# Kernel tuning notes

Hardware: AMD Instinct MI355X
Metric: run time of the kernel (lower is better)

## Reference

```python
import jax, jax.numpy as jnp
import numpy as np

B, CH, N = 4, 128, 4096
PC = CH // 2  # pos channels = 64


def setup_inputs() -> dict:
    key = jax.random.key(0)
    ks = jax.random.split(key, 6)
    s_p = 1.0 / np.sqrt(PC)
    s_v = 1.0 / np.sqrt(CH)
    return {
        "pos_bot": jax.random.normal(ks[0], (B, PC, N), dtype=jnp.float32),
        "corr_feats": jax.random.normal(ks[1], (B, CH, N), dtype=jnp.float32),
        "Wp": jax.random.uniform(ks[2], (PC, PC), jnp.float32, -s_p, s_p),
        "bp": jax.random.uniform(ks[3], (PC,), jnp.float32, -s_p, s_p),
        "Wv": jax.random.uniform(ks[4], (CH, CH), jnp.float32, -s_v, s_v),
        "bv": jax.random.uniform(ks[5], (CH,), jnp.float32, -s_v, s_v),
        "beta": jnp.asarray([1.0], dtype=jnp.float32),
    }


def reference(pos_bot, corr_feats, Wp, bp, Wv, bv, beta):
    # 1x1 Conv1d == per-position matmul over channels
    pos = jnp.einsum("oc,bcn->bon", Wp, pos_bot) + bp[None, :, None]      # [B,64,N]
    value = jnp.einsum("oc,bcn->bon", Wv, corr_feats) + bv[None, :, None]  # [B,128,N]

    x = jnp.transpose(pos, (0, 2, 1))  # [B,N,64]
    # squared euclidean pairwise distance: ||xi||^2 + ||xj||^2 - 2 xi.xj
    sq = jnp.sum(x * x, axis=-1)  # [B,N]
    d2 = sq[:, :, None] + sq[:, None, :] - 2.0 * jnp.einsum("bnd,bmd->bnm", x, x)
    d2 = jnp.maximum(d2, 0.0)
    kernel = jnp.exp(-d2 * beta[0])  # [B,N,N] Gaussian RBF

    equation_F = jnp.transpose(value, (0, 2, 1))  # [B,N,128]
    return kernel, equation_F
```

## Files before the change

kernel.cpp:

```cpp
#include <hip/hip_runtime.h>
#include <hip/hip_bf16.h>

typedef _Float16 f16x8 __attribute__((ext_vector_type(8)));
typedef _Float16 f16x4 __attribute__((ext_vector_type(4)));
typedef float    f32x4 __attribute__((ext_vector_type(4)));

constexpr int BB = 4;
constexpr int CH = 128;
constexpr int PC = 64;
constexpr int NN = 4096;

__global__ __launch_bounds__(256) void proj_pos_kernel(
    const float* __restrict__ pos_bot,
    const float* __restrict__ Wp,
    const float* __restrict__ bp,
    _Float16* __restrict__ xbuf,
    float*    __restrict__ sq)
{
    const int tid  = threadIdx.x;
    const int wid  = tid >> 6;
    const int lane = tid & 63;
    const int l15  = lane & 15;
    const int lg   = lane >> 4;
    const int b    = blockIdx.y;
    const int n    = blockIdx.x * 16 + l15;
    const int mt   = wid;

    f16x8 wf[2], pb[2];
#pragma unroll
    for (int ks = 0; ks < 2; ++ks) {
        const float* wp = Wp + (mt * 16 + l15) * PC + ks * 32 + lg * 8;
        f32x4 w0 = *reinterpret_cast<const f32x4*>(wp);
        f32x4 w1 = *reinterpret_cast<const f32x4*>(wp + 4);
        f16x8 f;
#pragma unroll
        for (int e = 0; e < 4; ++e) { f[e] = (_Float16)w0[e]; f[e + 4] = (_Float16)w1[e]; }
        wf[ks] = f;
        f16x8 g;
#pragma unroll
        for (int e = 0; e < 8; ++e) {
            const int c = ks * 32 + lg * 8 + e;
            g[e] = (_Float16)pos_bot[((size_t)(b * PC + c)) * NN + n];
        }
        pb[ks] = g;
    }

    f32x4 acc = {0.f, 0.f, 0.f, 0.f};
    acc = __builtin_amdgcn_mfma_f32_16x16x32_f16(wf[0], pb[0], acc, 0, 0, 0);
    acc = __builtin_amdgcn_mfma_f32_16x16x32_f16(wf[1], pb[1], acc, 0, 0, 0);

    float partial = 0.f;
    f16x4 h4;
#pragma unroll
    for (int r = 0; r < 4; ++r) {
        const int o = mt * 16 + lg * 4 + r;
        const float v = acc[r] + bp[o];
        const _Float16 h = (_Float16)v;
        h4[r] = h;
        const float hf = (float)h;
        partial = fmaf(hf, hf, partial);
    }
    *reinterpret_cast<f16x4*>(xbuf + ((size_t)(b * NN + n)) * PC + mt * 16 + lg * 4) = h4;

    partial += __shfl_xor(partial, 16);
    partial += __shfl_xor(partial, 32);
    __shared__ float psum[4][16];
    if (lane < 16) psum[wid][l15] = partial;
    __syncthreads();
    if (tid < 16)
        sq[b * NN + blockIdx.x * 16 + tid] =
            psum[0][tid] + psum[1][tid] + psum[2][tid] + psum[3][tid];
}

__global__ __launch_bounds__(256) void gram_kernel(
    const _Float16* __restrict__ xbuf,
    const float*    __restrict__ sq,
    const float*    __restrict__ beta,
    float*          __restrict__ out,
    const float*    __restrict__ corr,
    const float*    __restrict__ Wv,
    const float*    __restrict__ bv,
    float*          __restrict__ eqF)
{
    const int tid  = threadIdx.x;
    const int wid  = tid >> 6;
    const int lane = tid & 63;
    const int l15  = lane & 15;
    const int lg   = lane >> 4;

    if (blockIdx.z == BB) {
        const int blk = blockIdx.y * 32 + blockIdx.x;
        const int b   = blk >> 8;
        const int n   = (blk & 255) * 16 + l15;

        f16x8 cb[4];
#pragma unroll
        for (int ks = 0; ks < 4; ++ks) {
            f16x8 g;
#pragma unroll
            for (int e = 0; e < 8; ++e) {
                const int c = ks * 32 + lg * 8 + e;
                g[e] = (_Float16)corr[((size_t)(b * CH + c)) * NN + n];
            }
            cb[ks] = g;
        }
#pragma unroll
        for (int half = 0; half < 2; ++half) {
            const int ot = wid + half * 4;
            f32x4 acc = {0.f, 0.f, 0.f, 0.f};
#pragma unroll
            for (int ks = 0; ks < 4; ++ks) {
                const float* wv = Wv + (ot * 16 + l15) * CH + ks * 32 + lg * 8;
                f32x4 w0 = *reinterpret_cast<const f32x4*>(wv);
                f32x4 w1 = *reinterpret_cast<const f32x4*>(wv + 4);
                f16x8 f;
#pragma unroll
                for (int e = 0; e < 4; ++e) { f[e] = (_Float16)w0[e]; f[e + 4] = (_Float16)w1[e]; }
                acc = __builtin_amdgcn_mfma_f32_16x16x32_f16(f, cb[ks], acc, 0, 0, 0);
            }
            f32x4 o4;
#pragma unroll
            for (int r = 0; r < 4; ++r) o4[r] = acc[r] + bv[ot * 16 + lg * 4 + r];
            *reinterpret_cast<f32x4*>(eqF + ((size_t)(b * NN + n)) * CH + ot * 16 + lg * 4) = o4;
        }
        return;
    }

    const int wr = wid >> 1;
    const int wc = wid & 1;
    const int b  = blockIdx.z;
    const int ib = blockIdx.x * 128 + wr * 64;
    const int jb = blockIdx.y * 128 + wc * 64;

    const _Float16* xb = xbuf + (size_t)b * NN * PC;
    const f32x4 zero = {0.f, 0.f, 0.f, 0.f};

    f16x8 af[4][2], bf[4][2];
#pragma unroll
    for (int t = 0; t < 4; ++t)
#pragma unroll
        for (int ks = 0; ks < 2; ++ks) {
            af[t][ks] = *reinterpret_cast<const f16x8*>(
                xb + (size_t)(ib + t * 16 + l15) * PC + ks * 32 + lg * 8);
            bf[t][ks] = *reinterpret_cast<const f16x8*>(
                xb + (size_t)(jb + t * 16 + l15) * PC + ks * 32 + lg * 8);
        }

    f32x4 acc[4][4];
#pragma unroll
    for (int it = 0; it < 4; ++it)
#pragma unroll
        for (int jt = 0; jt < 4; ++jt) acc[it][jt] = zero;

#pragma unroll
    for (int ks = 0; ks < 2; ++ks)
#pragma unroll
        for (int it = 0; it < 4; ++it)
#pragma unroll
            for (int jt = 0; jt < 4; ++jt)
                acc[it][jt] = __builtin_amdgcn_mfma_f32_16x16x32_f16(
                    bf[jt][ks], af[it][ks], acc[it][jt], 0, 0, 0);

    const float* sqb = sq + (size_t)b * NN;
    const float bs   = -beta[0] * 1.44269504088896f;
    const float m2bs = -2.f * bs;

    f32x4 tj[4];
#pragma unroll
    for (int jt = 0; jt < 4; ++jt) {
        f32x4 s = *reinterpret_cast<const f32x4*>(sqb + jb + jt * 16 + lg * 4);
        tj[jt] = s * bs;
    }

#pragma unroll
    for (int it = 0; it < 4; ++it) {
        const int i   = ib + it * 16 + l15;
        const float ti = bs * sqb[i];
        float* orow = out + ((size_t)(b * NN + i)) * NN;
#pragma unroll
        for (int jt = 0; jt < 4; ++jt) {
            f32x4 v;
#pragma unroll
            for (int r = 0; r < 4; ++r) {
                float arg = fmaf(m2bs, acc[it][jt][r], ti + tj[jt][r]);
                arg = fminf(arg, 0.f);
                v[r] = __builtin_amdgcn_exp2f(arg);
            }
            *reinterpret_cast<f32x4*>(orow + jb + jt * 16 + lg * 4) = v;
        }
    }
}

extern "C" void kernel_launch(void* const* d_in, const int* in_sizes, int n_in,
                              void* d_out, int out_size, void* d_ws, size_t ws_size,
                              hipStream_t stream) {
    const float* pos_bot = (const float*)d_in[0];
    const float* corr    = (const float*)d_in[1];
    const float* Wp      = (const float*)d_in[2];
    const float* bp      = (const float*)d_in[3];
    const float* Wv      = (const float*)d_in[4];
    const float* bv      = (const float*)d_in[5];
    const float* beta    = (const float*)d_in[6];

    float* out = (float*)d_out;
    float* eqF = out + (size_t)BB * NN * NN;

    _Float16* xbuf = (_Float16*)d_ws;
    float* sq = (float*)((char*)d_ws + (size_t)BB * NN * PC * sizeof(_Float16));

    proj_pos_kernel<<<dim3(NN / 16, BB), 256, 0, stream>>>(pos_bot, Wp, bp, xbuf, sq);

    gram_kernel<<<dim3(NN / 128, NN / 128, BB + 1), 256, 0, stream>>>(
        xbuf, sq, beta, out, corr, Wv, bv, eqF);
}
```

Baseline: 79.95 us.

## Restructure gram kernel into row-strip blocks streaming column tiles

The value projection is split out of the fused gram launch into its own kernel. The gram kernel now gives each 512-thread block a 32-row strip, and each wave walks 512 columns in 16-wide tiles, prefetching the next tile's fp16 vectors and squared norms. The aim is full-row coalesced writes of the 256 MB output and less register pressure than the old 4x4 accumulator tiles. In exchange, each store is a scalar per lane rather than a vector store, and an extra kernel launch is added.

```diff
diff --git a/kernel.cpp b/kernel.cpp
--- a/kernel.cpp
+++ b/kernel.cpp
@@ -72,122 +72,123 @@
             psum[0][tid] + psum[1][tid] + psum[2][tid] + psum[3][tid];
 }
 
-__global__ __launch_bounds__(256) void gram_kernel(
-    const _Float16* __restrict__ xbuf,
-    const float*    __restrict__ sq,
-    const float*    __restrict__ beta,
-    float*          __restrict__ out,
-    const float*    __restrict__ corr,
-    const float*    __restrict__ Wv,
-    const float*    __restrict__ bv,
-    float*          __restrict__ eqF)
+__global__ __launch_bounds__(256) void proj_val_kernel(
+    const float* __restrict__ corr,
+    const float* __restrict__ Wv,
+    const float* __restrict__ bv,
+    float*       __restrict__ eqF)
 {
     const int tid  = threadIdx.x;
     const int wid  = tid >> 6;
     const int lane = tid & 63;
     const int l15  = lane & 15;
     const int lg   = lane >> 4;
-
-    if (blockIdx.z == BB) {
-        const int blk = blockIdx.y * 32 + blockIdx.x;
-        const int b   = blk >> 8;
-        const int n   = (blk & 255) * 16 + l15;
-
-        f16x8 cb[4];
+    const int b    = blockIdx.y;
+    const int n    = blockIdx.x * 16 + l15;
+
+    f16x8 cb[4];
+#pragma unroll
+    for (int ks = 0; ks < 4; ++ks) {
+        f16x8 g;
+#pragma unroll
+        for (int e = 0; e < 8; ++e) {
+            const int c = ks * 32 + lg * 8 + e;
+            g[e] = (_Float16)corr[((size_t)(b * CH + c)) * NN + n];
+        }
+        cb[ks] = g;
+    }
+#pragma unroll
+    for (int half = 0; half < 2; ++half) {
+        const int ot = wid + half * 4;
+        f32x4 acc = {0.f, 0.f, 0.f, 0.f};
 #pragma unroll
         for (int ks = 0; ks < 4; ++ks) {
-            f16x8 g;
-#pragma unroll
-            for (int e = 0; e < 8; ++e) {
-                const int c = ks * 32 + lg * 8 + e;
-                g[e] = (_Float16)corr[((size_t)(b * CH + c)) * NN + n];
-            }
-            cb[ks] = g;
-        }
-#pragma unroll
-        for (int half = 0; half < 2; ++half) {
-            const int ot = wid + half * 4;
-            f32x4 acc = {0.f, 0.f, 0.f, 0.f};
-#pragma unroll
-            for (int ks = 0; ks < 4; ++ks) {
-                const float* wv = Wv + (ot * 16 + l15) * CH + ks * 32 + lg * 8;
-                f32x4 w0 = *reinterpret_cast<const f32x4*>(wv);
-                f32x4 w1 = *reinterpret_cast<const f32x4*>(wv + 4);
-                f16x8 f;
-#pragma unroll
-                for (int e = 0; e < 4; ++e) { f[e] = (_Float16)w0[e]; f[e + 4] = (_Float16)w1[e]; }
-                acc = __builtin_amdgcn_mfma_f32_16x16x32_f16(f, cb[ks], acc, 0, 0, 0);
-            }
-            f32x4 o4;
-#pragma unroll
-            for (int r = 0; r < 4; ++r) o4[r] = acc[r] + bv[ot * 16 + lg * 4 + r];
-            *reinterpret_cast<f32x4*>(eqF + ((size_t)(b * NN + n)) * CH + ot * 16 + lg * 4) = o4;
-        }
-        return;
-    }
-
-    const int wr = wid >> 1;
-    const int wc = wid & 1;
-    const int b  = blockIdx.z;
-    const int ib = blockIdx.x * 128 + wr * 64;
-    const int jb = blockIdx.y * 128 + wc * 64;
-
-    const _Float16* xb = xbuf + (size_t)b * NN * PC;
-    const f32x4 zero = {0.f, 0.f, 0.f, 0.f};
-
-    f16x8 af[4][2], bf[4][2];
-#pragma unroll
-    for (int t = 0; t < 4; ++t)
-#pragma unroll
-        for (int ks = 0; ks < 2; ++ks) {
-            af[t][ks] = *reinterpret_cast<const f16x8*>(
-                xb + (size_t)(ib + t * 16 + l15) * PC + ks * 32 + lg * 8);
-            bf[t][ks] = *reinterpret_cast<const f16x8*>(
-                xb + (size_t)(jb + t * 16 + l15) * PC + ks * 32 + lg * 8);
-        }
-
-    f32x4 acc[4][4];
-#pragma unroll
-    for (int it = 0; it < 4; ++it)
-#pragma unroll
-        for (int jt = 0; jt < 4; ++jt) acc[it][jt] = zero;
-
-#pragma unroll
-    for (int ks = 0; ks < 2; ++ks)
-#pragma unroll
-        for (int it = 0; it < 4; ++it)
-#pragma unroll
-            for (int jt = 0; jt < 4; ++jt)
-                acc[it][jt] = __builtin_amdgcn_mfma_f32_16x16x32_f16(
-                    bf[jt][ks], af[it][ks], acc[it][jt], 0, 0, 0);
-
-    const float* sqb = sq + (size_t)b * NN;
+            const float* wv = Wv + (ot * 16 + l15) * CH + ks * 32 + lg * 8;
+            f32x4 w0 = *reinterpret_cast<const f32x4*>(wv);
+            f32x4 w1 = *reinterpret_cast<const f32x4*>(wv + 4);
+            f16x8 f;
+#pragma unroll
+            for (int e = 0; e < 4; ++e) { f[e] = (_Float16)w0[e]; f[e + 4] = (_Float16)w1[e]; }
+            acc = __builtin_amdgcn_mfma_f32_16x16x32_f16(f, cb[ks], acc, 0, 0, 0);
+        }
+        f32x4 o4;
+#pragma unroll
+        for (int r = 0; r < 4; ++r) o4[r] = acc[r] + bv[ot * 16 + lg * 4 + r];
+        *reinterpret_cast<f32x4*>(eqF + ((size_t)(b * NN + n)) * CH + ot * 16 + lg * 4) = o4;
+    }
+}
+
+__global__ __launch_bounds__(512) void gram_kernel(
+    const _Float16* __restrict__ xbuf,
+    const float*    __restrict__ sq,
+    const float*    __restrict__ beta,
+    float*          __restrict__ out)
+{
+    const int tid  = threadIdx.x;
+    const int wid  = tid >> 6;
+    const int lane = tid & 63;
+    const int l15  = lane & 15;
+    const int lg   = lane >> 4;
+    const int b    = blockIdx.y;
+    const int rb   = blockIdx.x * 32;
+
+    const _Float16* xb  = xbuf + (size_t)b * NN * PC;
+    const float*    sqb = sq + (size_t)b * NN;
+
+    f16x8 af[2][2];
+#pragma unroll
+    for (int it = 0; it < 2; ++it)
+#pragma unroll
+        for (int ks = 0; ks < 2; ++ks)
+            af[it][ks] = *reinterpret_cast<const f16x8*>(
+                xb + (size_t)(rb + it * 16 + l15) * PC + ks * 32 + lg * 8);
+
     const float bs   = -beta[0] * 1.44269504088896f;
     const float m2bs = -2.f * bs;
 
-    f32x4 tj[4];
-#pragma unroll
-    for (int jt = 0; jt < 4; ++jt) {
-        f32x4 s = *reinterpret_cast<const f32x4*>(sqb + jb + jt * 16 + lg * 4);
-        tj[jt] = s * bs;
-    }
-
-#pragma unroll
-    for (int it = 0; it < 4; ++it) {
-        const int i   = ib + it * 16 + l15;
-        const float ti = bs * sqb[i];
-        float* orow = out + ((size_t)(b * NN + i)) * NN;
-#pragma unroll
-        for (int jt = 0; jt < 4; ++jt) {
-            f32x4 v;
-#pragma unroll
-            for (int r = 0; r < 4; ++r) {
-                float arg = fmaf(m2bs, acc[it][jt][r], ti + tj[jt][r]);
-                arg = fminf(arg, 0.f);
-                v[r] = __builtin_amdgcn_exp2f(arg);
-            }
-            *reinterpret_cast<f32x4*>(orow + jb + jt * 16 + lg * 4) = v;
-        }
+    float ti[2][4];
+#pragma unroll
+    for (int it = 0; it < 2; ++it)
+#pragma unroll
+        for (int r = 0; r < 4; ++r)
+            ti[it][r] = bs * sqb[rb + it * 16 + lg * 4 + r];
+
+    const int jbase = wid * 512;
+
+    f16x8 b0, b1, n0, n1;
+    float tj, ntj;
+    {
+        const int j = jbase;
+        b0 = *reinterpret_cast<const f16x8*>(xb + (size_t)(j + l15) * PC + lg * 8);
+        b1 = *reinterpret_cast<const f16x8*>(xb + (size_t)(j + l15) * PC + 32 + lg * 8);
+        tj = bs * sqb[j + l15];
+    }
+
+    for (int jt = 0; jt < 32; ++jt) {
+        const int jn = jbase + (jt < 31 ? jt + 1 : 31) * 16;
+        n0 = *reinterpret_cast<const f16x8*>(xb + (size_t)(jn + l15) * PC + lg * 8);
+        n1 = *reinterpret_cast<const f16x8*>(xb + (size_t)(jn + l15) * PC + 32 + lg * 8);
+        ntj = bs * sqb[jn + l15];
+
+        f32x4 acc0 = {0.f, 0.f, 0.f, 0.f};
+        f32x4 acc1 = {0.f, 0.f, 0.f, 0.f};
+        acc0 = __builtin_amdgcn_mfma_f32_16x16x32_f16(af[0][0], b0, acc0, 0, 0, 0);
+        acc0 = __builtin_amdgcn_mfma_f32_16x16x32_f16(af[0][1], b1, acc0, 0, 0, 0);
+        acc1 = __builtin_amdgcn_mfma_f32_16x16x32_f16(af[1][0], b0, acc1, 0, 0, 0);
+        acc1 = __builtin_amdgcn_mfma_f32_16x16x32_f16(af[1][1], b1, acc1, 0, 0, 0);
+
+        const int j = jbase + jt * 16 + l15;
+#pragma unroll
+        for (int r = 0; r < 4; ++r) {
+            float a0 = fminf(fmaf(m2bs, acc0[r], ti[0][r] + tj), 0.f);
+            out[((size_t)(b * NN + rb + lg * 4 + r)) * NN + j] =
+                __builtin_amdgcn_exp2f(a0);
+            float a1 = fminf(fmaf(m2bs, acc1[r], ti[1][r] + tj), 0.f);
+            out[((size_t)(b * NN + rb + 16 + lg * 4 + r)) * NN + j] =
+                __builtin_amdgcn_exp2f(a1);
+        }
+
+        b0 = n0; b1 = n1; tj = ntj;
     }
 }
 
@@ -209,7 +210,6 @@
     float* sq = (float*)((char*)d_ws + (size_t)BB * NN * PC * sizeof(_Float16));
 
     proj_pos_kernel<<<dim3(NN / 16, BB), 256, 0, stream>>>(pos_bot, Wp, bp, xbuf, sq);
-
-    gram_kernel<<<dim3(NN / 128, NN / 128, BB + 1), 256, 0, stream>>>(
-        xbuf, sq, beta, out, corr, Wv, bv, eqF);
-}
+    proj_val_kernel<<<dim3(NN / 16, BB), 256, 0, stream>>>(corr, Wv, bv, eqF);
+    gram_kernel<<<dim3(NN / 32, BB), 512, 0, stream>>>(xbuf, sq, beta, out);
+}
```

Result: no change. 78.87 us (-1.4%).

## Stage gram tiles through LDS for full-row coalesced stores; move value proj to proj kernel

Applied to the files above, without the earlier changes.

The value projection moves out of the gram kernel into the first projection kernel, which now covers both position and value blocks. The gram kernel is retiled so each block covers 64 rows by 512 columns, with B fragments kept in registers across four 16-row slices. Each slice's exp results go through shared memory so every wave writes 2 KB contiguous row segments, instead of scattered 16-byte pieces across many rows. This targets write efficiency on the 256 MB kernel output, at the cost of extra shared-memory traffic and barriers per slice.

```diff
diff --git a/kernel.cpp b/kernel.cpp
--- a/kernel.cpp
+++ b/kernel.cpp
@@ -10,183 +10,186 @@
 constexpr int PC = 64;
 constexpr int NN = 4096;
 
-__global__ __launch_bounds__(256) void proj_pos_kernel(
+__global__ __launch_bounds__(256) void proj_kernel(
     const float* __restrict__ pos_bot,
+    const float* __restrict__ corr,
     const float* __restrict__ Wp,
     const float* __restrict__ bp,
+    const float* __restrict__ Wv,
+    const float* __restrict__ bv,
     _Float16* __restrict__ xbuf,
-    float*    __restrict__ sq)
+    float*    __restrict__ sq,
+    float*    __restrict__ eqF)
 {
     const int tid  = threadIdx.x;
     const int wid  = tid >> 6;
     const int lane = tid & 63;
     const int l15  = lane & 15;
     const int lg   = lane >> 4;
-    const int b    = blockIdx.y;
+    const int b    = blockIdx.y & 3;
     const int n    = blockIdx.x * 16 + l15;
-    const int mt   = wid;
-
-    f16x8 wf[2], pb[2];
-#pragma unroll
-    for (int ks = 0; ks < 2; ++ks) {
-        const float* wp = Wp + (mt * 16 + l15) * PC + ks * 32 + lg * 8;
-        f32x4 w0 = *reinterpret_cast<const f32x4*>(wp);
-        f32x4 w1 = *reinterpret_cast<const f32x4*>(wp + 4);
-        f16x8 f;
-#pragma unroll
-        for (int e = 0; e < 4; ++e) { f[e] = (_Float16)w0[e]; f[e + 4] = (_Float16)w1[e]; }
-        wf[ks] = f;
+
+    if ((blockIdx.y >> 2) == 0) {
+        const int mt = wid;
+        f16x8 wf[2], pb[2];
+#pragma unroll
+        for (int ks = 0; ks < 2; ++ks) {
+            const float* wp = Wp + (mt * 16 + l15) * PC + ks * 32 + lg * 8;
+            f32x4 w0 = *reinterpret_cast<const f32x4*>(wp);
+            f32x4 w1 = *reinterpret_cast<const f32x4*>(wp + 4);
+            f16x8 f;
+#pragma unroll
+            for (int e = 0; e < 4; ++e) { f[e] = (_Float16)w0[e]; f[e + 4] = (_Float16)w1[e]; }
+            wf[ks] = f;
+            f16x8 g;
+#pragma unroll
+            for (int e = 0; e < 8; ++e) {
+                const int c = ks * 32 + lg * 8 + e;
+                g[e] = (_Float16)pos_bot[((size_t)(b * PC + c)) * NN + n];
+            }
+            pb[ks] = g;
+        }
+
+        f32x4 acc = {0.f, 0.f, 0.f, 0.f};
+        acc = __builtin_amdgcn_mfma_f32_16x16x32_f16(wf[0], pb[0], acc, 0, 0, 0);
+        acc = __builtin_amdgcn_mfma_f32_16x16x32_f16(wf[1], pb[1], acc, 0, 0, 0);
+
+        float partial = 0.f;
+        f16x4 h4;
+#pragma unroll
+        for (int r = 0; r < 4; ++r) {
+            const int o = mt * 16 + lg * 4 + r;
+            const float v = acc[r] + bp[o];
+            const _Float16 h = (_Float16)v;
+            h4[r] = h;
+            const float hf = (float)h;
+            partial = fmaf(hf, hf, partial);
+        }
+        *reinterpret_cast<f16x4*>(xbuf + ((size_t)(b * NN + n)) * PC + mt * 16 + lg * 4) = h4;
+
+        partial += __shfl_xor(partial, 16);
+        partial += __shfl_xor(partial, 32);
+        __shared__ float psum[4][16];
+        if (lane < 16) psum[wid][l15] = partial;
+        __syncthreads();
+        if (tid < 16)
+            sq[b * NN + blockIdx.x * 16 + tid] =
+                psum[0][tid] + psum[1][tid] + psum[2][tid] + psum[3][tid];
+        return;
+    }
+
+    f16x8 cb[4];
+#pragma unroll
+    for (int ks = 0; ks < 4; ++ks) {
         f16x8 g;
 #pragma unroll
         for (int e = 0; e < 8; ++e) {
             const int c = ks * 32 + lg * 8 + e;
-            g[e] = (_Float16)pos_bot[((size_t)(b * PC + c)) * NN + n];
-        }
-        pb[ks] = g;
-    }
-
-    f32x4 acc = {0.f, 0.f, 0.f, 0.f};
-    acc = __builtin_amdgcn_mfma_f32_16x16x32_f16(wf[0], pb[0], acc, 0, 0, 0);
-    acc = __builtin_amdgcn_mfma_f32_16x16x32_f16(wf[1], pb[1], acc, 0, 0, 0);
-
-    float partial = 0.f;
-    f16x4 h4;
-#pragma unroll
-    for (int r = 0; r < 4; ++r) {
-        const int o = mt * 16 + lg * 4 + r;
-        const float v = acc[r] + bp[o];
-        const _Float16 h = (_Float16)v;
-        h4[r] = h;
-        const float hf = (float)h;
-        partial = fmaf(hf, hf, partial);
-    }
-    *reinterpret_cast<f16x4*>(xbuf + ((size_t)(b * NN + n)) * PC + mt * 16 + lg * 4) = h4;
-
-    partial += __shfl_xor(partial, 16);
-    partial += __shfl_xor(partial, 32);
-    __shared__ float psum[4][16];
-    if (lane < 16) psum[wid][l15] = partial;
-    __syncthreads();
-    if (tid < 16)
-        sq[b * NN + blockIdx.x * 16 + tid] =
-            psum[0][tid] + psum[1][tid] + psum[2][tid] + psum[3][tid];
+            g[e] = (_Float16)corr[((size_t)(b * CH + c)) * NN + n];
+        }
+        cb[ks] = g;
+    }
+#pragma unroll
+    for (int half = 0; half < 2; ++half) {
+        const int ot = wid + half * 4;
+        f32x4 acc = {0.f, 0.f, 0.f, 0.f};
+#pragma unroll
+        for (int ks = 0; ks < 4; ++ks) {
+            const float* wv = Wv + (ot * 16 + l15) * CH + ks * 32 + lg * 8;
+            f32x4 w0 = *reinterpret_cast<const f32x4*>(wv);
+            f32x4 w1 = *reinterpret_cast<const f32x4*>(wv + 4);
+            f16x8 f;
+#pragma unroll
+            for (int e = 0; e < 4; ++e) { f[e] = (_Float16)w0[e]; f[e + 4] = (_Float16)w1[e]; }
+            acc = __builtin_amdgcn_mfma_f32_16x16x32_f16(f, cb[ks], acc, 0, 0, 0);
+        }
+        f32x4 o4;
+#pragma unroll
+        for (int r = 0; r < 4; ++r) o4[r] = acc[r] + bv[ot * 16 + lg * 4 + r];
+        *reinterpret_cast<f32x4*>(eqF + ((size_t)(b * NN + n)) * CH + ot * 16 + lg * 4) = o4;
+    }
 }
 
 __global__ __launch_bounds__(256) void gram_kernel(
     const _Float16* __restrict__ xbuf,
     const float*    __restrict__ sq,
     const float*    __restrict__ beta,
-    float*          __restrict__ out,
-    const float*    __restrict__ corr,
-    const float*    __restrict__ Wv,
-    const float*    __restrict__ bv,
-    float*          __restrict__ eqF)
+    float*          __restrict__ out)
 {
     const int tid  = threadIdx.x;
     const int wid  = tid >> 6;
     const int lane = tid & 63;
     const int l15  = lane & 15;
     const int lg   = lane >> 4;
-
-    if (blockIdx.z == BB) {
-        const int blk = blockIdx.y * 32 + blockIdx.x;
-        const int b   = blk >> 8;
-        const int n   = (blk & 255) * 16 + l15;
-
-        f16x8 cb[4];
-#pragma unroll
-        for (int ks = 0; ks < 4; ++ks) {
-            f16x8 g;
-#pragma unroll
-            for (int e = 0; e < 8; ++e) {
-                const int c = ks * 32 + lg * 8 + e;
-                g[e] = (_Float16)corr[((size_t)(b * CH + c)) * NN + n];
-            }
-            cb[ks] = g;
-        }
-#pragma unroll
-        for (int half = 0; half < 2; ++half) {
-            const int ot = wid + half * 4;
-            f32x4 acc = {0.f, 0.f, 0.f, 0.f};
-#pragma unroll
-            for (int ks = 0; ks < 4; ++ks) {
-                const float* wv = Wv + (ot * 16 + l15) * CH + ks * 32 + lg * 8;
-                f32x4 w0 = *reinterpret_cast<const f32x4*>(wv);
-                f32x4 w1 = *reinterpret_cast<const f32x4*>(wv + 4);
-                f16x8 f;
-#pragma unroll
-                for (int e = 0; e < 4; ++e) { f[e] = (_Float16)w0[e]; f[e + 4] = (_Float16)w1[e]; }
-                acc = __builtin_amdgcn_mfma_f32_16x16x32_f16(f, cb[ks], acc, 0, 0, 0);
-            }
-            f32x4 o4;
-#pragma unroll
-            for (int r = 0; r < 4; ++r) o4[r] = acc[r] + bv[ot * 16 + lg * 4 + r];
-            *reinterpret_cast<f32x4*>(eqF + ((size_t)(b * NN + n)) * CH + ot * 16 + lg * 4) = o4;
-        }
-        return;
-    }
-
-    const int wr = wid >> 1;
-    const int wc = wid & 1;
-    const int b  = blockIdx.z;
-    const int ib = blockIdx.x * 128 + wr * 64;
-    const int jb = blockIdx.y * 128 + wc * 64;
-
-    const _Float16* xb = xbuf + (size_t)b * NN * PC;
-    const f32x4 zero = {0.f, 0.f, 0.f, 0.f};
-
-    f16x8 af[4][2], bf[4][2];
-#pragma unroll
-    for (int t = 0; t < 4; ++t)
-#pragma unroll
-        for (int ks = 0; ks < 2; ++ks) {
-            af[t][ks] = *reinterpret_cast<const f16x8*>(
-                xb + (size_t)(ib + t * 16 + l15) * PC + ks * 32 + lg * 8);
-            bf[t][ks] = *reinterpret_cast<const f16x8*>(
-                xb + (size_t)(jb + t * 16 + l15) * PC + ks * 32 + lg * 8);
-        }
-
-    f32x4 acc[4][4];
-#pragma unroll
-    for (int it = 0; it < 4; ++it)
-#pragma unroll
-        for (int jt = 0; jt < 4; ++jt) acc[it][jt] = zero;
-
-#pragma unroll
-    for (int ks = 0; ks < 2; ++ks)
-#pragma unroll
-        for (int it = 0; it < 4; ++it)
-#pragma unroll
-            for (int jt = 0; jt < 4; ++jt)
-                acc[it][jt] = __builtin_amdgcn_mfma_f32_16x16x32_f16(
-                    bf[jt][ks], af[it][ks], acc[it][jt], 0, 0, 0);
-
-    const float* sqb = sq + (size_t)b * NN;
+    const int b    = blockIdx.z;
+    const int jb   = blockIdx.x * 512;
+    const int rb   = blockIdx.y * 64;
+
+    const _Float16* xb  = xbuf + (size_t)b * NN * PC;
+    const float*    sqb = sq + (size_t)b * NN;
+
     const float bs   = -beta[0] * 1.44269504088896f;
     const float m2bs = -2.f * bs;
 
-    f32x4 tj[4];
-#pragma unroll
-    for (int jt = 0; jt < 4; ++jt) {
-        f32x4 s = *reinterpret_cast<const f32x4*>(sqb + jb + jt * 16 + lg * 4);
-        tj[jt] = s * bs;
-    }
-
-#pragma unroll
-    for (int it = 0; it < 4; ++it) {
-        const int i   = ib + it * 16 + l15;
-        const float ti = bs * sqb[i];
-        float* orow = out + ((size_t)(b * NN + i)) * NN;
-#pragma unroll
-        for (int jt = 0; jt < 4; ++jt) {
-            f32x4 v;
+    f16x8 bf[8][2];
+    float tj[8];
+#pragma unroll
+    for (int jtf = 0; jtf < 8; ++jtf) {
+        const int j = jb + wid * 128 + jtf * 16 + l15;
+#pragma unroll
+        for (int ks = 0; ks < 2; ++ks)
+            bf[jtf][ks] = *reinterpret_cast<const f16x8*>(
+                xb + (size_t)j * PC + ks * 32 + lg * 8);
+        tj[jtf] = bs * sqb[j];
+    }
+
+    __shared__ float lds[16][516];
+
+    for (int sl = 0; sl < 4; ++sl) {
+        const int ibase = rb + sl * 16;
+
+        const f16x8 af0 = *reinterpret_cast<const f16x8*>(
+            xb + (size_t)(ibase + l15) * PC + lg * 8);
+        const f16x8 af1 = *reinterpret_cast<const f16x8*>(
+            xb + (size_t)(ibase + l15) * PC + 32 + lg * 8);
+
+        f32x4 acc[8];
+#pragma unroll
+        for (int jtf = 0; jtf < 8; ++jtf) {
+            f32x4 z = {0.f, 0.f, 0.f, 0.f};
+            acc[jtf] = __builtin_amdgcn_mfma_f32_16x16x32_f16(af0, bf[jtf][0], z, 0, 0, 0);
+        }
+#pragma unroll
+        for (int jtf = 0; jtf < 8; ++jtf)
+            acc[jtf] = __builtin_amdgcn_mfma_f32_16x16x32_f16(af1, bf[jtf][1], acc[jtf], 0, 0, 0);
+
+        float ti[4];
+#pragma unroll
+        for (int r = 0; r < 4; ++r) ti[r] = bs * sqb[ibase + lg * 4 + r];
+
+        if (sl) __syncthreads();
+
+#pragma unroll
+        for (int jtf = 0; jtf < 8; ++jtf) {
 #pragma unroll
             for (int r = 0; r < 4; ++r) {
-                float arg = fmaf(m2bs, acc[it][jt][r], ti + tj[jt][r]);
-                arg = fminf(arg, 0.f);
-                v[r] = __builtin_amdgcn_exp2f(arg);
+                float arg = fminf(fmaf(m2bs, acc[jtf][r], ti[r] + tj[jtf]), 0.f);
+                lds[lg * 4 + r][wid * 128 + jtf * 16 + l15] =
+                    __builtin_amdgcn_exp2f(arg);
             }
-            *reinterpret_cast<f32x4*>(orow + jb + jt * 16 + lg * 4) = v;
+        }
+        __syncthreads();
+
+#pragma unroll
+        for (int rr = 0; rr < 4; ++rr) {
+            const int row = rr * 4 + wid;
+            float* orow = out + ((size_t)(b * NN + ibase + row)) * NN + jb;
+#pragma unroll
+            for (int c2 = 0; c2 < 2; ++c2) {
+                const int col = c2 * 256 + lane * 4;
+                *reinterpret_cast<f32x4*>(orow + col) =
+                    *reinterpret_cast<const f32x4*>(&lds[row][col]);
+            }
         }
     }
 }
@@ -208,8 +211,9 @@
     _Float16* xbuf = (_Float16*)d_ws;
     float* sq = (float*)((char*)d_ws + (size_t)BB * NN * PC * sizeof(_Float16));
 
-    proj_pos_kernel<<<dim3(NN / 16, BB), 256, 0, stream>>>(pos_bot, Wp, bp, xbuf, sq);
-
-    gram_kernel<<<dim3(NN / 128, NN / 128, BB + 1), 256, 0, stream>>>(
-        xbuf, sq, beta, out, corr, Wv, bv, eqF);
+    proj_kernel<<<dim3(NN / 16, 2 * BB), 256, 0, stream>>>(
+        pos_bot, corr, Wp, bp, Wv, bv, xbuf, sq, eqF);
+
+    gram_kernel<<<dim3(NN / 512, NN / 64, BB), 256, 0, stream>>>(
+        xbuf, sq, beta, out);
 }
```

New measurement: 72.05 us. 1.11x faster.
